# Kernel tuning notes

Measured on AMD Instinct MI355X. Metric: run time of the kernel, lower is better.

The kernel has to match this reference:

```python
import jax, jax.numpy as jnp
import numpy as np

N_NODES = 100000
N_EDGES = 1600000
IN_DIM = 128
EMB_DIM = 128
NUM_EDGE_EMB = 4
LN_EPS = 1e-5


def setup_inputs() -> dict:
    key = jax.random.key(0)
    ks = jax.random.split(key, 8)
    x = jax.random.normal(ks[0], (N_NODES, IN_DIM), dtype=jnp.float32)
    edge_index = jax.random.randint(ks[1], (2, N_EDGES), 0, N_NODES, dtype=jnp.int64)
    edge_attr = jax.random.randint(ks[2], (N_EDGES,), 0, NUM_EDGE_EMB, dtype=jnp.int64)
    # learned params
    edge_emb = jax.random.normal(ks[3], (NUM_EDGE_EMB, IN_DIM), dtype=jnp.float32)
    eps = jnp.zeros((), dtype=jnp.float32)  # GINEConv train_eps init 0
    s1 = 1.0 / np.sqrt(IN_DIM)
    W1 = jax.random.uniform(ks[4], (IN_DIM, EMB_DIM), jnp.float32, -s1, s1)
    b1 = jnp.zeros((EMB_DIM,), jnp.float32)
    ln_g = jnp.ones((EMB_DIM,), jnp.float32)
    ln_b = jnp.zeros((EMB_DIM,), jnp.float32)
    s2 = 1.0 / np.sqrt(EMB_DIM)
    W2 = jax.random.uniform(ks[5], (EMB_DIM, EMB_DIM), jnp.float32, -s2, s2)
    b2 = jnp.zeros((EMB_DIM,), jnp.float32)
    return {"x": x, "edge_index": edge_index, "edge_attr": edge_attr,
            "edge_emb": edge_emb, "eps": eps, "W1": W1, "b1": b1,
            "ln_g": ln_g, "ln_b": ln_b, "W2": W2, "b2": b2}


def reference(x, edge_index, edge_attr, edge_emb, eps, W1, b1, ln_g, ln_b, W2, b2):
    src, dst = edge_index[0], edge_index[1]
    # message: relu(x_j + e_ji), gathered per edge [E, D]
    msg = jax.nn.relu(x[src] + edge_emb[edge_attr])
    # scatter-add into destination nodes [N, D]
    agg = jax.ops.segment_sum(msg, dst, num_segments=x.shape[0])
    h = (1.0 + eps) * x + agg
    # MLP: Linear -> LayerNorm -> ReLU -> Linear
    h1 = h @ W1 + b1
    mu = jnp.mean(h1, axis=-1, keepdims=True)
    var = jnp.var(h1, axis=-1, keepdims=True)
    h1 = (h1 - mu) * jax.lax.rsqrt(var + LN_EPS) * ln_g + ln_b
    h1 = jax.nn.relu(h1)
    return h1 @ W2 + b2
```

## Files before the change

### kernel.cpp

```cpp
#include <hip/hip_runtime.h>
#include <hip/hip_fp16.h>

#define N_NODES 100000
#define N_EDGES 1600000
#define DIM 128
#define NBUK 391
#define EPB 4096
#define NBLK 391
#define NCNT (NBUK * NBLK)
#define NSC 150
#define CAPB 5120

typedef __attribute__((ext_vector_type(8))) short short8v;
typedef __attribute__((ext_vector_type(4))) float f32x4;
typedef _Float16 h2 __attribute__((ext_vector_type(2)));

__device__ __forceinline__ unsigned short f2bf(float f) {
    unsigned u = __float_as_uint(f);
    unsigned r = u + 0x7FFFu + ((u >> 16) & 1u);
    return (unsigned short)(r >> 16);
}
__device__ __forceinline__ float bf2f(unsigned short b) {
    return __uint_as_float(((unsigned)b) << 16);
}

__global__ __launch_bounds__(256) void hist2_conv(
    const int* __restrict__ ei, int* __restrict__ cnts,
    const float* __restrict__ x, ushort* __restrict__ xh, int do_conv)
{
    __shared__ int cnt[NBUK];
    for (int i = threadIdx.x; i < NBUK; i += 256) cnt[i] = 0;

    if (do_conv) {
        for (int i = blockIdx.x * 256 + threadIdx.x; i < N_NODES * DIM / 4;
             i += NBLK * 256) {
            float4 v = ((const float4*)x)[i];
            ushort4 o;
            o.x = __half_as_ushort(__float2half(v.x));
            o.y = __half_as_ushort(__float2half(v.y));
            o.z = __half_as_ushort(__float2half(v.z));
            o.w = __half_as_ushort(__float2half(v.w));
            ((ushort4*)xh)[i] = o;
        }
    }
    __syncthreads();

    int e0 = blockIdx.x * EPB;
    int e1 = min(e0 + EPB, N_EDGES);
    for (int e = e0 + threadIdx.x; e < e1; e += 256)
        atomicAdd(&cnt[ei[N_EDGES + e] >> 8], 1);
    __syncthreads();
    for (int b = threadIdx.x; b < NBUK; b += 256)
        cnts[b * NBLK + blockIdx.x] = cnt[b];
}

__global__ __launch_bounds__(256) void scanA(
    const int* __restrict__ cnts, int* __restrict__ ebase, int* __restrict__ bsums)
{
    __shared__ int s[256];
    int t = threadIdx.x;
    int base = blockIdx.x * 1024 + t * 4;
    int v0 = (base + 0 < NCNT) ? cnts[base + 0] : 0;
    int v1 = (base + 1 < NCNT) ? cnts[base + 1] : 0;
    int v2 = (base + 2 < NCNT) ? cnts[base + 2] : 0;
    int v3 = (base + 3 < NCNT) ? cnts[base + 3] : 0;
    int sum = v0 + v1 + v2 + v3;
    s[t] = sum;
    __syncthreads();
    for (int off = 1; off < 256; off <<= 1) {
        int x = (t >= off) ? s[t - off] : 0;
        __syncthreads();
        s[t] += x;
        __syncthreads();
    }
    int excl = s[t] - sum;
    if (base + 0 < NCNT) ebase[base + 0] = excl;  excl += v0;
    if (base + 1 < NCNT) ebase[base + 1] = excl;  excl += v1;
    if (base + 2 < NCNT) ebase[base + 2] = excl;  excl += v2;
    if (base + 3 < NCNT) ebase[base + 3] = excl;
    if (t == 255) bsums[blockIdx.x] = s[255];
}

__global__ __launch_bounds__(256) void scanB(int* __restrict__ bsums)
{
    __shared__ int s[256];
    int t = threadIdx.x;
    int v = (t < NSC) ? bsums[t] : 0;
    s[t] = v;
    __syncthreads();
    for (int off = 1; off < 256; off <<= 1) {
        int x = (t >= off) ? s[t - off] : 0;
        __syncthreads();
        s[t] += x;
        __syncthreads();
    }
    if (t < NSC) bsums[t] = s[t] - v;
}

__global__ __launch_bounds__(256) void scanC(
    int* __restrict__ ebase, const int* __restrict__ bsums, int* __restrict__ bk)
{
    int i = blockIdx.x * 256 + threadIdx.x;
    if (i < NCNT) {
        int v = ebase[i] + bsums[i >> 10];
        ebase[i] = v;
        if (i % NBLK == 0) bk[i / NBLK] = v;
    }
    if (i == 0) bk[NBUK] = N_EDGES;
}

__global__ __launch_bounds__(256) void prep_w(
    const float* __restrict__ W1, const float* __restrict__ W2,
    ushort* __restrict__ wf1, ushort* __restrict__ wf2)
{
    int o = blockIdx.x * 256 + threadIdx.x;
    int lane = (o >> 3) & 63;
    int j = o & 7;
    int frag = o >> 9;
    int kt = frag >> 3, nt = frag & 7;
    int k = kt * 32 + (lane >> 4) * 8 + j;
    int n = nt * 16 + (lane & 15);
    wf1[o] = f2bf(W1[k * DIM + n]);
    wf2[o] = f2bf(W2[k * DIM + n]);
}

__global__ __launch_bounds__(256) void pass2_scatter(
    const int* __restrict__ ei, const int* __restrict__ ea,
    const int* __restrict__ ebase, int* __restrict__ ebuf)
{
    __shared__ int cnt[NBUK];
    __shared__ int mybase[NBUK];
    for (int i = threadIdx.x; i < NBUK; i += 256) {
        cnt[i] = 0;
        mybase[i] = ebase[i * NBLK + blockIdx.x];
    }
    __syncthreads();
    int e0 = blockIdx.x * EPB;
    int e1 = min(e0 + EPB, N_EDGES);
    for (int e = e0 + threadIdx.x; e < e1; e += 256) {
        int src = ei[e];
        int dst = ei[N_EDGES + e];
        int at  = ea[e];
        int pay = src | (at << 17) | ((dst & 255) << 19);
        int b   = dst >> 8;
        int r   = atomicAdd(&cnt[b], 1);
        ebuf[mybase[b] + r] = pay;
    }
}

__global__ __launch_bounds__(512) void phaseB_sort(
    const int* __restrict__ bk, const int* __restrict__ ebuf,
    int* __restrict__ rs, int* __restrict__ col)
{
    __shared__ int eb[CAPB];
    __shared__ int deg[256];
    __shared__ int cur[256];
    __shared__ int s[256];

    int b = blockIdx.x;
    int lo = bk[b], hi = bk[b + 1];
    int n_e = min(hi - lo, CAPB);
    int t = threadIdx.x;

    for (int i = t; i < n_e; i += 512) eb[i] = ebuf[lo + i];
    if (t < 256) deg[t] = 0;
    __syncthreads();

    for (int i = t; i < n_e; i += 512)
        atomicAdd(&deg[((unsigned)eb[i] >> 19)], 1);
    __syncthreads();

    if (t < 256) s[t] = deg[t];
    __syncthreads();
    for (int off = 1; off < 256; off <<= 1) {
        int xv = 0;
        if (t < 256 && t >= off) xv = s[t - off];
        __syncthreads();
        if (t < 256) s[t] += xv;
        __syncthreads();
    }
    if (t < 256) {
        int v = deg[t];
        int excl = s[t] - v;
        cur[t] = excl;
        int node = b * 256 + t;
        if (node < N_NODES) rs[node] = lo + excl;
    }
    if (b == NBUK - 1 && t == 0) rs[N_NODES] = N_EDGES;
    __syncthreads();

    for (int i = t; i < n_e; i += 512) {
        int pk = eb[i];
        int p = atomicAdd(&cur[(unsigned)pk >> 19], 1);
        col[lo + p] = pk;
    }
}

template<int HI>
__device__ __forceinline__ float h2acc(h2 m2, float acc) {
#if __has_builtin(__builtin_amdgcn_fdot2)
    h2 b;
    b[0] = (_Float16)(HI ? 0.f : 1.f);
    b[1] = (_Float16)(HI ? 1.f : 0.f);
    return __builtin_amdgcn_fdot2(m2, b, acc, false);
#else
    return acc + (float)m2[HI];
#endif
}

__device__ __forceinline__ void edge_acc(
    int pkv, int c, const unsigned* embh, float* acc, uint4 xv)
{
    const uint4 ev = *(const uint4*)&embh[((((unsigned)pkv >> 17) & 3) << 6) | (c << 2)];
    unsigned xs[4] = {xv.x, xv.y, xv.z, xv.w};
    unsigned es[4] = {ev.x, ev.y, ev.z, ev.w};
    const h2 z2 = (h2)(_Float16)0;
    #pragma unroll
    for (int j = 0; j < 4; ++j) {
        h2 a = __builtin_bit_cast(h2, xs[j]);
        h2 b = __builtin_bit_cast(h2, es[j]);
        h2 m2 = __builtin_elementwise_max(a + b, z2);
        acc[2 * j]     = h2acc<0>(m2, acc[2 * j]);
        acc[2 * j + 1] = h2acc<1>(m2, acc[2 * j + 1]);
    }
}

__global__ __launch_bounds__(256) void gather_f16(
    const float* __restrict__ x,
    const ushort* __restrict__ xh,
    const float* __restrict__ emb,
    const int* __restrict__ rs,
    const int* __restrict__ col,
    const float* __restrict__ eps_p,
    ushort* __restrict__ hhi, ushort* __restrict__ hlo)
{
    __shared__ unsigned embh[4 * DIM / 2];
    {
        float2 f = ((const float2*)emb)[threadIdx.x & 255];
        __half2 h = __floats2half2_rn(f.x, f.y);
        embh[threadIdx.x & 255] = __builtin_bit_cast(unsigned, h);
    }
    __syncthreads();

    int gid = blockIdx.x * 256 + threadIdx.x;
    int n = gid >> 4;
    if (n >= N_NODES) return;
    int c = gid & 15;

    int start = rs[n], end = rs[n + 1];
    float acc[8] = {0.f, 0.f, 0.f, 0.f, 0.f, 0.f, 0.f, 0.f};

    int p = start;
    for (; p + 4 <= end; p += 4) {
        int pk[4];
        uint4 xv[4];
        #pragma unroll
        for (int u = 0; u < 4; ++u) pk[u] = col[p + u];
        #pragma unroll
        for (int u = 0; u < 4; ++u)
            xv[u] = ((const uint4*)xh)[((pk[u] & 0x1FFFF) << 4) | c];
        #pragma unroll
        for (int u = 0; u < 4; ++u)
            edge_acc(pk[u], c, embh, acc, xv[u]);
    }
    for (; p < end; ++p) {
        int pkv = col[p];
        uint4 xv = ((const uint4*)xh)[((pkv & 0x1FFFF) << 4) | c];
        edge_acc(pkv, c, embh, acc, xv);
    }

    float epsv = 1.0f + eps_p[0];
    float4 xa = ((const float4*)(x + (size_t)n * DIM))[c * 2];
    float4 xb = ((const float4*)(x + (size_t)n * DIM))[c * 2 + 1];
    float o[8];
    o[0] = epsv * xa.x + acc[0];
    o[1] = epsv * xa.y + acc[1];
    o[2] = epsv * xa.z + acc[2];
    o[3] = epsv * xa.w + acc[3];
    o[4] = epsv * xb.x + acc[4];
    o[5] = epsv * xb.y + acc[5];
    o[6] = epsv * xb.z + acc[6];
    o[7] = epsv * xb.w + acc[7];

    unsigned hiw[4], low[4];
    #pragma unroll
    for (int j = 0; j < 4; ++j) {
        unsigned short h0 = f2bf(o[2 * j]);
        unsigned short h1 = f2bf(o[2 * j + 1]);
        unsigned short l0 = f2bf(o[2 * j] - bf2f(h0));
        unsigned short l1 = f2bf(o[2 * j + 1] - bf2f(h1));
        hiw[j] = (unsigned)h0 | ((unsigned)h1 << 16);
        low[j] = (unsigned)l0 | ((unsigned)l1 << 16);
    }
    ((uint4*)(hhi + (size_t)n * DIM))[c] = make_uint4(hiw[0], hiw[1], hiw[2], hiw[3]);
    ((uint4*)(hlo + (size_t)n * DIM))[c] = make_uint4(low[0], low[1], low[2], low[3]);
}

__device__ __forceinline__ float4 sel4(
    float4 e0, float4 e1, float4 e2, float4 e3, int at)
{
    float4 a = (at & 1) ? e1 : e0;
    float4 b = (at & 1) ? e3 : e2;
    return (at & 2) ? b : a;
}

__device__ __forceinline__ void write_split(
    ushort* hhi, ushort* hlo, int n, int c, float4 o)
{
    ushort4 hi4, lo4;
    hi4.x = f2bf(o.x); lo4.x = f2bf(o.x - bf2f(hi4.x));
    hi4.y = f2bf(o.y); lo4.y = f2bf(o.y - bf2f(hi4.y));
    hi4.z = f2bf(o.z); lo4.z = f2bf(o.z - bf2f(hi4.z));
    hi4.w = f2bf(o.w); lo4.w = f2bf(o.w - bf2f(hi4.w));
    ((ushort4*)(hhi + (size_t)n * DIM))[c] = hi4;
    ((ushort4*)(hlo + (size_t)n * DIM))[c] = lo4;
}

__global__ __launch_bounds__(256) void gather_f32(
    const float* __restrict__ x,
    const float* __restrict__ emb,
    const int* __restrict__ rs,
    const int* __restrict__ col,
    const float* __restrict__ eps_p,
    ushort* __restrict__ hhi, ushort* __restrict__ hlo)
{
    int gid = blockIdx.x * 256 + threadIdx.x;
    int n = gid >> 5;
    if (n >= N_NODES) return;
    int c = gid & 31;

    float4 er0 = ((const float4*)(emb + 0 * DIM))[c];
    float4 er1 = ((const float4*)(emb + 1 * DIM))[c];
    float4 er2 = ((const float4*)(emb + 2 * DIM))[c];
    float4 er3 = ((const float4*)(emb + 3 * DIM))[c];

    int start = rs[n], end = rs[n + 1];
    float4 acc = make_float4(0.f, 0.f, 0.f, 0.f);

    int p = start;
    for (; p + 4 <= end; p += 4) {
        int pk[4];
        float4 xv[4];
        #pragma unroll
        for (int u = 0; u < 4; ++u) pk[u] = col[p + u];
        #pragma unroll
        for (int u = 0; u < 4; ++u)
            xv[u] = ((const float4*)(x + (size_t)(pk[u] & 0x1FFFF) * DIM))[c];
        #pragma unroll
        for (int u = 0; u < 4; ++u) {
            float4 ev = sel4(er0, er1, er2, er3, ((unsigned)pk[u] >> 17) & 3);
            acc.x += fmaxf(xv[u].x + ev.x, 0.f);
            acc.y += fmaxf(xv[u].y + ev.y, 0.f);
            acc.z += fmaxf(xv[u].z + ev.z, 0.f);
            acc.w += fmaxf(xv[u].w + ev.w, 0.f);
        }
    }
    for (; p < end; ++p) {
        int pk = col[p];
        float4 xv = ((const float4*)(x + (size_t)(pk & 0x1FFFF) * DIM))[c];
        float4 ev = sel4(er0, er1, er2, er3, ((unsigned)pk >> 17) & 3);
        acc.x += fmaxf(xv.x + ev.x, 0.f);
        acc.y += fmaxf(xv.y + ev.y, 0.f);
        acc.z += fmaxf(xv.z + ev.z, 0.f);
        acc.w += fmaxf(xv.w + ev.w, 0.f);
    }

    float epsv = 1.0f + eps_p[0];
    float4 xn = ((const float4*)(x + (size_t)n * DIM))[c];
    float4 o;
    o.x = epsv * xn.x + acc.x;
    o.y = epsv * xn.y + acc.y;
    o.z = epsv * xn.z + acc.z;
    o.w = epsv * xn.w + acc.w;
    write_split(hhi, hlo, n, c, o);
}

__global__ __launch_bounds__(256) void fused_mlp(
    const ushort* __restrict__ hhi, const ushort* __restrict__ hlo,
    const ushort* __restrict__ wf1, const ushort* __restrict__ wf2,
    const float* __restrict__ b1,
    const float* __restrict__ lng, const float* __restrict__ lnb,
    const float* __restrict__ b2,
    float* __restrict__ out)
{
    __shared__ short w1s[DIM * DIM];
    __shared__ short w2s[DIM * DIM];
    __shared__ short scr[4 * 16 * DIM];

    #pragma unroll
    for (int i = 0; i < 8; ++i) {
        int idx = i * 256 + threadIdx.x;
        ((uint4*)w1s)[idx] = ((const uint4*)wf1)[idx];
        ((uint4*)w2s)[idx] = ((const uint4*)wf2)[idx];
    }
    __syncthreads();

    const int w  = threadIdx.x >> 6;
    const int l  = threadIdx.x & 63;
    const int lc = l & 15;
    const int lr = l >> 4;

    const int rbase = blockIdx.x * 64 + w * 16;
    const int arow = min(rbase + lc, N_NODES - 1);
    const ushort* hph = hhi + (size_t)arow * DIM;
    const ushort* hpl = hlo + (size_t)arow * DIM;

    float g[8], bb[8], bi1[8], bi2[8];
    #pragma unroll
    for (int nt = 0; nt < 8; ++nt) {
        g[nt]  = lng[nt * 16 + lc];
        bb[nt] = lnb[nt * 16 + lc];
        bi1[nt] = b1[nt * 16 + lc];
        bi2[nt] = b2[nt * 16 + lc];
    }

    f32x4 acc[8];
    #pragma unroll
    for (int nt = 0; nt < 8; ++nt)
        acc[nt] = (f32x4){bi1[nt], bi1[nt], bi1[nt], bi1[nt]};

    #pragma unroll
    for (int kt = 0; kt < 4; ++kt) {
        short8v ahi = *(const short8v*)(hph + kt * 32 + lr * 8);
        short8v alo = *(const short8v*)(hpl + kt * 32 + lr * 8);
        #pragma unroll
        for (int nt = 0; nt < 8; ++nt) {
            short8v bf = *(const short8v*)&w1s[((kt * 8 + nt) * 64 + l) * 8];
            acc[nt] = __builtin_amdgcn_mfma_f32_16x16x32_bf16(ahi, bf, acc[nt], 0, 0, 0);
            acc[nt] = __builtin_amdgcn_mfma_f32_16x16x32_bf16(alo, bf, acc[nt], 0, 0, 0);
        }
    }

    #pragma unroll
    for (int r = 0; r < 4; ++r) {
        float s1 = 0.f, s2 = 0.f;
        #pragma unroll
        for (int nt = 0; nt < 8; ++nt) { float v = acc[nt][r]; s1 += v; s2 += v * v; }
        s1 += __shfl_xor(s1, 1);  s2 += __shfl_xor(s2, 1);
        s1 += __shfl_xor(s1, 2);  s2 += __shfl_xor(s2, 2);
        s1 += __shfl_xor(s1, 4);  s2 += __shfl_xor(s2, 4);
        s1 += __shfl_xor(s1, 8);  s2 += __shfl_xor(s2, 8);
        float mu  = s1 * (1.0f / DIM);
        float var = s2 * (1.0f / DIM) - mu * mu;
        float rsd = rsqrtf(var + 1e-5f);
        int row = lr * 4 + r;
        #pragma unroll
        for (int nt = 0; nt < 8; ++nt) {
            float v = (acc[nt][r] - mu) * rsd * g[nt] + bb[nt];
            v = fmaxf(v, 0.f);
            int cidx = nt * 16 + lc;
            scr[w * 2048 + row * 128 + (((cidx >> 3) ^ row) << 3) + (cidx & 7)]
                = (short)f2bf(v);
        }
    }

    f32x4 acc2[8];
    #pragma unroll
    for (int nt = 0; nt < 8; ++nt)
        acc2[nt] = (f32x4){bi2[nt], bi2[nt], bi2[nt], bi2[nt]};

    #pragma unroll
    for (int kt = 0; kt < 4; ++kt) {
        short8v a2 = *(const short8v*)&scr[w * 2048 + lc * 128 + (((kt * 4 + lr) ^ lc) << 3)];
        #pragma unroll
        for (int nt = 0; nt < 8; ++nt) {
            short8v bf = *(const short8v*)&w2s[((kt * 8 + nt) * 64 + l) * 8];
            acc2[nt] = __builtin_amdgcn_mfma_f32_16x16x32_bf16(a2, bf, acc2[nt], 0, 0, 0);
        }
    }

    #pragma unroll
    for (int r = 0; r < 4; ++r) {
        int orow = rbase + lr * 4 + r;
        if (orow < N_NODES) {
            #pragma unroll
            for (int nt = 0; nt < 8; ++nt)
                out[(size_t)orow * DIM + nt * 16 + lc] = acc2[nt][r];
        }
    }
}

extern "C" void kernel_launch(void* const* d_in, const int* in_sizes, int n_in,
                              void* d_out, int out_size, void* d_ws, size_t ws_size,
                              hipStream_t stream) {
    const float* x    = (const float*)d_in[0];
    const int*   ei   = (const int*)d_in[1];
    const int*   ea   = (const int*)d_in[2];
    const float* emb  = (const float*)d_in[3];
    const float* epsp = (const float*)d_in[4];
    const float* W1   = (const float*)d_in[5];
    const float* b1   = (const float*)d_in[6];
    const float* lng  = (const float*)d_in[7];
    const float* lnb  = (const float*)d_in[8];
    const float* W2   = (const float*)d_in[9];
    const float* b2   = (const float*)d_in[10];
    float* out = (float*)d_out;

    char* ws = (char*)d_ws;
    int* rs    = (int*)(ws);
    int* bk    = (int*)(ws +   400128);
    int* bsums = (int*)(ws +   401792);
    int* cnts  = (int*)(ws +   402816);
    ushort* wf1 = (ushort*)(ws + 402816);
    ushort* wf2 = (ushort*)(ws + 435584);
    int* ebase = (int*)(ws +  1014400);
    int* col   = (int*)(ws +  1625984);
    int* ebuf  = (int*)(ws +  8025984);
    ushort* hhi = (ushort*)(ws + 8025984);
    ushort* hlo = (ushort*)(ws + 33625984);
    ushort* xh  = (ushort*)(ws + 59225984);
    const size_t NEED = 59225984 + (size_t)N_NODES * DIM * 2;

    const int use_f16 = (ws_size >= NEED) ? 1 : 0;

    hist2_conv<<<NBLK, 256, 0, stream>>>(ei, cnts, x, xh, use_f16);
    scanA<<<NSC, 256, 0, stream>>>(cnts, ebase, bsums);
    scanB<<<1, 256, 0, stream>>>(bsums);
    scanC<<<(NCNT + 255) / 256, 256, 0, stream>>>(ebase, bsums, bk);
    prep_w<<<64, 256, 0, stream>>>(W1, W2, wf1, wf2);
    pass2_scatter<<<NBLK, 256, 0, stream>>>(ei, ea, ebase, ebuf);
    phaseB_sort<<<NBUK, 512, 0, stream>>>(bk, ebuf, rs, col);

    if (use_f16) {
        gather_f16<<<(N_NODES * 16 + 255) / 256, 256, 0, stream>>>(
            x, xh, emb, rs, col, epsp, hhi, hlo);
    } else {
        gather_f32<<<(N_NODES * 32) / 256, 256, 0, stream>>>(
            x, emb, rs, col, epsp, hhi, hlo);
    }

    fused_mlp<<<(N_NODES + 63) / 64, 256, 0, stream>>>(
        hhi, hlo, wf1, wf2, b1, lng, lnb, b2, out);
}
```

Baseline: 159.6 us.

## Fuse per-bucket sort into gather kernel with 128-node buckets

```diff
diff --git a/kernel.cpp b/kernel.cpp
--- a/kernel.cpp
+++ b/kernel.cpp
@@ -4,12 +4,12 @@
 #define N_NODES 100000
 #define N_EDGES 1600000
 #define DIM 128
-#define NBUK 391
+#define NBUK 782
 #define EPB 4096
 #define NBLK 391
 #define NCNT (NBUK * NBLK)
-#define NSC 150
-#define CAPB 5120
+#define NSC 299
+#define CAPB 2720
 
 typedef __attribute__((ext_vector_type(8))) short short8v;
 typedef __attribute__((ext_vector_type(4))) float f32x4;
@@ -48,14 +48,14 @@
     int e0 = blockIdx.x * EPB;
     int e1 = min(e0 + EPB, N_EDGES);
     for (int e = e0 + threadIdx.x; e < e1; e += 256)
-        atomicAdd(&cnt[ei[N_EDGES + e] >> 8], 1);
+        atomicAdd(&cnt[ei[N_EDGES + e] >> 7], 1);
     __syncthreads();
     for (int b = threadIdx.x; b < NBUK; b += 256)
         cnts[b * NBLK + blockIdx.x] = cnt[b];
 }
 
 __global__ __launch_bounds__(256) void scanA(
-    const int* __restrict__ cnts, int* __restrict__ ebase, int* __restrict__ bsums)
+    int* __restrict__ cnts, int* __restrict__ bsums)
 {
     __shared__ int s[256];
     int t = threadIdx.x;
@@ -74,21 +74,21 @@
         __syncthreads();
     }
     int excl = s[t] - sum;
-    if (base + 0 < NCNT) ebase[base + 0] = excl;  excl += v0;
-    if (base + 1 < NCNT) ebase[base + 1] = excl;  excl += v1;
-    if (base + 2 < NCNT) ebase[base + 2] = excl;  excl += v2;
-    if (base + 3 < NCNT) ebase[base + 3] = excl;
+    if (base + 0 < NCNT) cnts[base + 0] = excl;  excl += v0;
+    if (base + 1 < NCNT) cnts[base + 1] = excl;  excl += v1;
+    if (base + 2 < NCNT) cnts[base + 2] = excl;  excl += v2;
+    if (base + 3 < NCNT) cnts[base + 3] = excl;
     if (t == 255) bsums[blockIdx.x] = s[255];
 }
 
-__global__ __launch_bounds__(256) void scanB(int* __restrict__ bsums)
-{
-    __shared__ int s[256];
+__global__ __launch_bounds__(512) void scanB(int* __restrict__ bsums)
+{
+    __shared__ int s[512];
     int t = threadIdx.x;
     int v = (t < NSC) ? bsums[t] : 0;
     s[t] = v;
     __syncthreads();
-    for (int off = 1; off < 256; off <<= 1) {
+    for (int off = 1; off < 512; off <<= 1) {
         int x = (t >= off) ? s[t - off] : 0;
         __syncthreads();
         s[t] += x;
@@ -97,8 +97,10 @@
     if (t < NSC) bsums[t] = s[t] - v;
 }
 
-__global__ __launch_bounds__(256) void scanC(
-    int* __restrict__ ebase, const int* __restrict__ bsums, int* __restrict__ bk)
+__global__ __launch_bounds__(256) void scanC_prepw(
+    int* __restrict__ ebase, const int* __restrict__ bsums, int* __restrict__ bk,
+    const float* __restrict__ W1, const float* __restrict__ W2,
+    ushort* __restrict__ wf1, ushort* __restrict__ wf2)
 {
     int i = blockIdx.x * 256 + threadIdx.x;
     if (i < NCNT) {
@@ -107,21 +109,17 @@
         if (i % NBLK == 0) bk[i / NBLK] = v;
     }
     if (i == 0) bk[NBUK] = N_EDGES;
-}
-
-__global__ __launch_bounds__(256) void prep_w(
-    const float* __restrict__ W1, const float* __restrict__ W2,
-    ushort* __restrict__ wf1, ushort* __restrict__ wf2)
-{
-    int o = blockIdx.x * 256 + threadIdx.x;
-    int lane = (o >> 3) & 63;
-    int j = o & 7;
-    int frag = o >> 9;
-    int kt = frag >> 3, nt = frag & 7;
-    int k = kt * 32 + (lane >> 4) * 8 + j;
-    int n = nt * 16 + (lane & 15);
-    wf1[o] = f2bf(W1[k * DIM + n]);
-    wf2[o] = f2bf(W2[k * DIM + n]);
+
+    if (i < DIM * DIM) {
+        int lane = (i >> 3) & 63;
+        int j = i & 7;
+        int frag = i >> 9;
+        int kt = frag >> 3, nt = frag & 7;
+        int k = kt * 32 + (lane >> 4) * 8 + j;
+        int n = nt * 16 + (lane & 15);
+        wf1[i] = f2bf(W1[k * DIM + n]);
+        wf2[i] = f2bf(W2[k * DIM + n]);
+    }
 }
 
 __global__ __launch_bounds__(256) void pass2_scatter(
@@ -141,58 +139,10 @@
         int src = ei[e];
         int dst = ei[N_EDGES + e];
         int at  = ea[e];
-        int pay = src | (at << 17) | ((dst & 255) << 19);
-        int b   = dst >> 8;
+        int pay = src | (at << 17) | ((dst & 127) << 19);
+        int b   = dst >> 7;
         int r   = atomicAdd(&cnt[b], 1);
         ebuf[mybase[b] + r] = pay;
-    }
-}
-
-__global__ __launch_bounds__(512) void phaseB_sort(
-    const int* __restrict__ bk, const int* __restrict__ ebuf,
-    int* __restrict__ rs, int* __restrict__ col)
-{
-    __shared__ int eb[CAPB];
-    __shared__ int deg[256];
-    __shared__ int cur[256];
-    __shared__ int s[256];
-
-    int b = blockIdx.x;
-    int lo = bk[b], hi = bk[b + 1];
-    int n_e = min(hi - lo, CAPB);
-    int t = threadIdx.x;
-
-    for (int i = t; i < n_e; i += 512) eb[i] = ebuf[lo + i];
-    if (t < 256) deg[t] = 0;
-    __syncthreads();
-
-    for (int i = t; i < n_e; i += 512)
-        atomicAdd(&deg[((unsigned)eb[i] >> 19)], 1);
-    __syncthreads();
-
-    if (t < 256) s[t] = deg[t];
-    __syncthreads();
-    for (int off = 1; off < 256; off <<= 1) {
-        int xv = 0;
-        if (t < 256 && t >= off) xv = s[t - off];
-        __syncthreads();
-        if (t < 256) s[t] += xv;
-        __syncthreads();
-    }
-    if (t < 256) {
-        int v = deg[t];
-        int excl = s[t] - v;
-        cur[t] = excl;
-        int node = b * 256 + t;
-        if (node < N_NODES) rs[node] = lo + excl;
-    }
-    if (b == NBUK - 1 && t == 0) rs[N_NODES] = N_EDGES;
-    __syncthreads();
-
-    for (int i = t; i < n_e; i += 512) {
-        int pk = eb[i];
-        int p = atomicAdd(&cur[(unsigned)pk >> 19], 1);
-        col[lo + p] = pk;
     }
 }
 
@@ -225,154 +175,132 @@
     }
 }
 
-__global__ __launch_bounds__(256) void gather_f16(
-    const float* __restrict__ x,
-    const ushort* __restrict__ xh,
-    const float* __restrict__ emb,
-    const int* __restrict__ rs,
-    const int* __restrict__ col,
-    const float* __restrict__ eps_p,
+template<int USE16>
+__global__ __launch_bounds__(512) void sort_gather(
+    const int* __restrict__ bk, const int* __restrict__ ebuf,
+    const float* __restrict__ x, const ushort* __restrict__ xh,
+    const float* __restrict__ emb, const float* __restrict__ eps_p,
     ushort* __restrict__ hhi, ushort* __restrict__ hlo)
 {
-    __shared__ unsigned embh[4 * DIM / 2];
-    {
-        float2 f = ((const float2*)emb)[threadIdx.x & 255];
-        __half2 h = __floats2half2_rn(f.x, f.y);
-        embh[threadIdx.x & 255] = __builtin_bit_cast(unsigned, h);
-    }
-    __syncthreads();
-
-    int gid = blockIdx.x * 256 + threadIdx.x;
-    int n = gid >> 4;
-    if (n >= N_NODES) return;
-    int c = gid & 15;
-
-    int start = rs[n], end = rs[n + 1];
-    float acc[8] = {0.f, 0.f, 0.f, 0.f, 0.f, 0.f, 0.f, 0.f};
-
-    int p = start;
-    for (; p + 4 <= end; p += 4) {
-        int pk[4];
-        uint4 xv[4];
+    __shared__ int eb[CAPB];
+    __shared__ int col_l[CAPB];
+    __shared__ int deg[128], sc[128], cur[128];
+    __shared__ unsigned embh[256];
+    __shared__ float femb[512];
+
+    const int b = blockIdx.x;
+    const int t = threadIdx.x;
+    const int lo = bk[b];
+    const int n_e = min(bk[b + 1] - lo, CAPB);
+
+    if (t < 256) {
+        float2 f = ((const float2*)emb)[t];
+        if (USE16) {
+            __half2 h = __floats2half2_rn(f.x, f.y);
+            embh[t] = __builtin_bit_cast(unsigned, h);
+        } else {
+            femb[2 * t] = f.x;
+            femb[2 * t + 1] = f.y;
+        }
+    }
+    if (t < 128) deg[t] = 0;
+    for (int i = t; i < n_e; i += 512) eb[i] = ebuf[lo + i];
+    __syncthreads();
+
+    for (int i = t; i < n_e; i += 512)
+        atomicAdd(&deg[((unsigned)eb[i] >> 19) & 127], 1);
+    __syncthreads();
+
+    if (t < 128) sc[t] = deg[t];
+    __syncthreads();
+    for (int off = 1; off < 128; off <<= 1) {
+        int v = 0;
+        if (t < 128 && t >= off) v = sc[t - off];
+        __syncthreads();
+        if (t < 128) sc[t] += v;
+        __syncthreads();
+    }
+    if (t < 128) cur[t] = sc[t] - deg[t];
+    __syncthreads();
+
+    for (int i = t; i < n_e; i += 512) {
+        int pk = eb[i];
+        int p = atomicAdd(&cur[((unsigned)pk >> 19) & 127], 1);
+        col_l[p] = pk;
+    }
+    __syncthreads();
+
+    const int g = t >> 4, c = t & 15;
+    const float epsv = 1.0f + eps_p[0];
+
+    for (int ln = g; ln < 128; ln += 32) {
+        int n = b * 128 + ln;
+        if (n >= N_NODES) break;
+        int start = sc[ln] - deg[ln], end = sc[ln];
+        float acc[8] = {0.f, 0.f, 0.f, 0.f, 0.f, 0.f, 0.f, 0.f};
+
+        if (USE16) {
+            int p = start;
+            for (; p + 4 <= end; p += 4) {
+                int pk[4];
+                uint4 xv[4];
+                #pragma unroll
+                for (int u = 0; u < 4; ++u) pk[u] = col_l[p + u];
+                #pragma unroll
+                for (int u = 0; u < 4; ++u)
+                    xv[u] = ((const uint4*)xh)[((pk[u] & 0x1FFFF) << 4) | c];
+                #pragma unroll
+                for (int u = 0; u < 4; ++u)
+                    edge_acc(pk[u], c, embh, acc, xv[u]);
+            }
+            for (; p < end; ++p) {
+                int pkv = col_l[p];
+                uint4 xv = ((const uint4*)xh)[((pkv & 0x1FFFF) << 4) | c];
+                edge_acc(pkv, c, embh, acc, xv);
+            }
+        } else {
+            for (int p = start; p < end; ++p) {
+                int pk = col_l[p];
+                const float* xr = x + (size_t)(pk & 0x1FFFF) * DIM;
+                float4 xa = ((const float4*)xr)[c * 2];
+                float4 xb = ((const float4*)xr)[c * 2 + 1];
+                const float* er = &femb[(((unsigned)pk >> 17) & 3) * DIM + c * 8];
+                acc[0] += fmaxf(xa.x + er[0], 0.f);
+                acc[1] += fmaxf(xa.y + er[1], 0.f);
+                acc[2] += fmaxf(xa.z + er[2], 0.f);
+                acc[3] += fmaxf(xa.w + er[3], 0.f);
+                acc[4] += fmaxf(xb.x + er[4], 0.f);
+                acc[5] += fmaxf(xb.y + er[5], 0.f);
+                acc[6] += fmaxf(xb.z + er[6], 0.f);
+                acc[7] += fmaxf(xb.w + er[7], 0.f);
+            }
+        }
+
+        float4 xa = ((const float4*)(x + (size_t)n * DIM))[c * 2];
+        float4 xb = ((const float4*)(x + (size_t)n * DIM))[c * 2 + 1];
+        float o[8];
+        o[0] = epsv * xa.x + acc[0];
+        o[1] = epsv * xa.y + acc[1];
+        o[2] = epsv * xa.z + acc[2];
+        o[3] = epsv * xa.w + acc[3];
+        o[4] = epsv * xb.x + acc[4];
+        o[5] = epsv * xb.y + acc[5];
+        o[6] = epsv * xb.z + acc[6];
+        o[7] = epsv * xb.w + acc[7];
+
+        unsigned hiw[4], low[4];
         #pragma unroll
-        for (int u = 0; u < 4; ++u) pk[u] = col[p + u];
-        #pragma unroll
-        for (int u = 0; u < 4; ++u)
-            xv[u] = ((const uint4*)xh)[((pk[u] & 0x1FFFF) << 4) | c];
-        #pragma unroll
-        for (int u = 0; u < 4; ++u)
-            edge_acc(pk[u], c, embh, acc, xv[u]);
-    }
-    for (; p < end; ++p) {
-        int pkv = col[p];
-        uint4 xv = ((const uint4*)xh)[((pkv & 0x1FFFF) << 4) | c];
-        edge_acc(pkv, c, embh, acc, xv);
-    }
-
-    float epsv = 1.0f + eps_p[0];
-    float4 xa = ((const float4*)(x + (size_t)n * DIM))[c * 2];
-    float4 xb = ((const float4*)(x + (size_t)n * DIM))[c * 2 + 1];
-    float o[8];
-    o[0] = epsv * xa.x + acc[0];
-    o[1] = epsv * xa.y + acc[1];
-    o[2] = epsv * xa.z + acc[2];
-    o[3] = epsv * xa.w + acc[3];
-    o[4] = epsv * xb.x + acc[4];
-    o[5] = epsv * xb.y + acc[5];
-    o[6] = epsv * xb.z + acc[6];
-    o[7] = epsv * xb.w + acc[7];
-
-    unsigned hiw[4], low[4];
-    #pragma unroll
-    for (int j = 0; j < 4; ++j) {
-        unsigned short h0 = f2bf(o[2 * j]);
-        unsigned short h1 = f2bf(o[2 * j + 1]);
-        unsigned short l0 = f2bf(o[2 * j] - bf2f(h0));
-        unsigned short l1 = f2bf(o[2 * j + 1] - bf2f(h1));
-        hiw[j] = (unsigned)h0 | ((unsigned)h1 << 16);
-        low[j] = (unsigned)l0 | ((unsigned)l1 << 16);
-    }
-    ((uint4*)(hhi + (size_t)n * DIM))[c] = make_uint4(hiw[0], hiw[1], hiw[2], hiw[3]);
-    ((uint4*)(hlo + (size_t)n * DIM))[c] = make_uint4(low[0], low[1], low[2], low[3]);
-}
-
-__device__ __forceinline__ float4 sel4(
-    float4 e0, float4 e1, float4 e2, float4 e3, int at)
-{
-    float4 a = (at & 1) ? e1 : e0;
-    float4 b = (at & 1) ? e3 : e2;
-    return (at & 2) ? b : a;
-}
-
-__device__ __forceinline__ void write_split(
-    ushort* hhi, ushort* hlo, int n, int c, float4 o)
-{
-    ushort4 hi4, lo4;
-    hi4.x = f2bf(o.x); lo4.x = f2bf(o.x - bf2f(hi4.x));
-    hi4.y = f2bf(o.y); lo4.y = f2bf(o.y - bf2f(hi4.y));
-    hi4.z = f2bf(o.z); lo4.z = f2bf(o.z - bf2f(hi4.z));
-    hi4.w = f2bf(o.w); lo4.w = f2bf(o.w - bf2f(hi4.w));
-    ((ushort4*)(hhi + (size_t)n * DIM))[c] = hi4;
-    ((ushort4*)(hlo + (size_t)n * DIM))[c] = lo4;
-}
-
-__global__ __launch_bounds__(256) void gather_f32(
-    const float* __restrict__ x,
-    const float* __restrict__ emb,
-    const int* __restrict__ rs,
-    const int* __restrict__ col,
-    const float* __restrict__ eps_p,
-    ushort* __restrict__ hhi, ushort* __restrict__ hlo)
-{
-    int gid = blockIdx.x * 256 + threadIdx.x;
-    int n = gid >> 5;
-    if (n >= N_NODES) return;
-    int c = gid & 31;
-
-    float4 er0 = ((const float4*)(emb + 0 * DIM))[c];
-    float4 er1 = ((const float4*)(emb + 1 * DIM))[c];
-    float4 er2 = ((const float4*)(emb + 2 * DIM))[c];
-    float4 er3 = ((const float4*)(emb + 3 * DIM))[c];
-
-    int start = rs[n], end = rs[n + 1];
-    float4 acc = make_float4(0.f, 0.f, 0.f, 0.f);
-
-    int p = start;
-    for (; p + 4 <= end; p += 4) {
-        int pk[4];
-        float4 xv[4];
-        #pragma unroll
-        for (int u = 0; u < 4; ++u) pk[u] = col[p + u];
-        #pragma unroll
-        for (int u = 0; u < 4; ++u)
-            xv[u] = ((const float4*)(x + (size_t)(pk[u] & 0x1FFFF) * DIM))[c];
-        #pragma unroll
-        for (int u = 0; u < 4; ++u) {
-            float4 ev = sel4(er0, er1, er2, er3, ((unsigned)pk[u] >> 17) & 3);
-            acc.x += fmaxf(xv[u].x + ev.x, 0.f);
-            acc.y += fmaxf(xv[u].y + ev.y, 0.f);
-            acc.z += fmaxf(xv[u].z + ev.z, 0.f);
-            acc.w += fmaxf(xv[u].w + ev.w, 0.f);
-        }
-    }
-    for (; p < end; ++p) {
-        int pk = col[p];
-        float4 xv = ((const float4*)(x + (size_t)(pk & 0x1FFFF) * DIM))[c];
-        float4 ev = sel4(er0, er1, er2, er3, ((unsigned)pk >> 17) & 3);
-        acc.x += fmaxf(xv.x + ev.x, 0.f);
-        acc.y += fmaxf(xv.y + ev.y, 0.f);
-        acc.z += fmaxf(xv.z + ev.z, 0.f);
-        acc.w += fmaxf(xv.w + ev.w, 0.f);
-    }
-
-    float epsv = 1.0f + eps_p[0];
-    float4 xn = ((const float4*)(x + (size_t)n * DIM))[c];
-    float4 o;
-    o.x = epsv * xn.x + acc.x;
-    o.y = epsv * xn.y + acc.y;
-    o.z = epsv * xn.z + acc.z;
-    o.w = epsv * xn.w + acc.w;
-    write_split(hhi, hlo, n, c, o);
+        for (int j = 0; j < 4; ++j) {
+            unsigned short h0 = f2bf(o[2 * j]);
+            unsigned short h1 = f2bf(o[2 * j + 1]);
+            unsigned short l0 = f2bf(o[2 * j] - bf2f(h0));
+            unsigned short l1 = f2bf(o[2 * j + 1] - bf2f(h1));
+            hiw[j] = (unsigned)h0 | ((unsigned)h1 << 16);
+            low[j] = (unsigned)l0 | ((unsigned)l1 << 16);
+        }
+        ((uint4*)(hhi + (size_t)n * DIM))[c] = make_uint4(hiw[0], hiw[1], hiw[2], hiw[3]);
+        ((uint4*)(hlo + (size_t)n * DIM))[c] = make_uint4(low[0], low[1], low[2], low[3]);
+    }
 }
 
 __global__ __launch_bounds__(256) void fused_mlp(
@@ -497,15 +425,12 @@
     float* out = (float*)d_out;
 
     char* ws = (char*)d_ws;
-    int* rs    = (int*)(ws);
-    int* bk    = (int*)(ws +   400128);
-    int* bsums = (int*)(ws +   401792);
-    int* cnts  = (int*)(ws +   402816);
-    ushort* wf1 = (ushort*)(ws + 402816);
-    ushort* wf2 = (ushort*)(ws + 435584);
-    int* ebase = (int*)(ws +  1014400);
-    int* col   = (int*)(ws +  1625984);
-    int* ebuf  = (int*)(ws +  8025984);
+    int* bk     = (int*)(ws);
+    int* bsums  = (int*)(ws + 4096);
+    ushort* wf1 = (ushort*)(ws + 8192);
+    ushort* wf2 = (ushort*)(ws + 40960);
+    int* cnts   = (int*)(ws + 81920);
+    int* ebuf   = (int*)(ws + 1310720);
     ushort* hhi = (ushort*)(ws + 8025984);
     ushort* hlo = (ushort*)(ws + 33625984);
     ushort* xh  = (ushort*)(ws + 59225984);
@@ -514,19 +439,18 @@
     const int use_f16 = (ws_size >= NEED) ? 1 : 0;
 
     hist2_conv<<<NBLK, 256, 0, stream>>>(ei, cnts, x, xh, use_f16);
-    scanA<<<NSC, 256, 0, stream>>>(cnts, ebase, bsums);
-    scanB<<<1, 256, 0, stream>>>(bsums);
-    scanC<<<(NCNT + 255) / 256, 256, 0, stream>>>(ebase, bsums, bk);
-    prep_w<<<64, 256, 0, stream>>>(W1, W2, wf1, wf2);
-    pass2_scatter<<<NBLK, 256, 0, stream>>>(ei, ea, ebase, ebuf);
-    phaseB_sort<<<NBUK, 512, 0, stream>>>(bk, ebuf, rs, col);
+    scanA<<<NSC, 256, 0, stream>>>(cnts, bsums);
+    scanB<<<1, 512, 0, stream>>>(bsums);
+    scanC_prepw<<<(NCNT + 255) / 256, 256, 0, stream>>>(
+        cnts, bsums, bk, W1, W2, wf1, wf2);
+    pass2_scatter<<<NBLK, 256, 0, stream>>>(ei, ea, cnts, ebuf);
 
     if (use_f16) {
-        gather_f16<<<(N_NODES * 16 + 255) / 256, 256, 0, stream>>>(
-            x, xh, emb, rs, col, epsp, hhi, hlo);
+        sort_gather<1><<<NBUK, 512, 0, stream>>>(
+            bk, ebuf, x, xh, emb, epsp, hhi, hlo);
     } else {
-        gather_f32<<<(N_NODES * 32) / 256, 256, 0, stream>>>(
-            x, emb, rs, col, epsp, hhi, hlo);
+        sort_gather<0><<<NBUK, 512, 0, stream>>>(
+            bk, ebuf, x, xh, emb, epsp, hhi, hlo);
     }
 
     fused_mlp<<<(N_NODES + 63) / 64, 256, 0, stream>>>(
```

Measured after the change: 158.8 us. About the same (-0.5%).
